# Optimization experiments

Measured on AMD Instinct MI355X. Metric: run time of the kernel, lower is better.

The kernel has to match this reference:

```python
import jax, jax.numpy as jnp
import numpy as np

BS, QLEN, KLEN = 2, 64, 64
N_HEADS, D_KV = 8, 64
INNER = N_HEADS * D_KV  # 512
VOCAB = 4096


def _layernorm(x, g, b, eps=1e-6):
    m = jnp.mean(x, axis=-1, keepdims=True)
    v = jnp.mean(jnp.square(x - m), axis=-1, keepdims=True)
    return (x - m) * jax.lax.rsqrt(v + eps) * g + b


def _l2norm(x, eps=1e-12):
    sq = jnp.sum(jnp.square(x), axis=-1, keepdims=True)
    return x * jax.lax.rsqrt(jnp.maximum(sq, eps))


def setup_inputs() -> dict:
    key = jax.random.key(0)
    ks = jax.random.split(key, 8)
    d = {
        'query': jax.random.normal(ks[0], (BS, QLEN, INNER), jnp.float32),
        'key': jax.random.normal(ks[1], (BS, KLEN, INNER), jnp.float32),
        'q_position_embeddings': jax.random.normal(ks[2], (BS, QLEN, INNER), jnp.float32),
        'k_position_embeddings': jax.random.normal(ks[3], (BS, KLEN, INNER), jnp.float32),
        'wi_w': jax.random.normal(ks[4], (2 * INNER, INNER), jnp.float32) / np.sqrt(2 * INNER),
        'vq_dict': jax.random.normal(ks[5], (VOCAB, D_KV), jnp.float32) * np.sqrt(2.0 / (VOCAB + D_KV)),
        'vq_ln_g': jnp.ones((D_KV,), jnp.float32),
        'vq_ln_b': jnp.zeros((D_KV,), jnp.float32),
        'vq_o_w': jax.random.normal(ks[6], (D_KV, D_KV), jnp.float32) / np.sqrt(D_KV),
        'ln_g': jnp.ones((D_KV,), jnp.float32),
        'ln_b': jnp.zeros((D_KV,), jnp.float32),
    }
    return d


def reference(query, key, q_position_embeddings, k_position_embeddings,
              wi_w, vq_dict, vq_ln_g, vq_ln_b, vq_o_w, ln_g, ln_b):
    bs, qlen, dim = query.shape
    klen = key.shape[1]

    q = query + q_position_embeddings
    k = key + k_position_embeddings
    # wi(concat([q, 0])) == q @ wi_w[:dim]; wi(concat([0, k])) == k @ wi_w[dim:]
    q_proj = jnp.einsum('bqd,de->bqe', q, wi_w[:dim])   # [bs, qlen, inner]
    k_proj = jnp.einsum('bkd,de->bke', k, wi_w[dim:])   # [bs, klen, inner]

    # pairwise outer sum -> [bs, qlen, klen, inner] -> tokens of size d_kv
    rcr = q_proj[:, :, None, :] + k_proj[:, None, :, :]
    y = rcr.reshape(bs, qlen * klen * N_HEADS, D_KV)

    # --- VectorQuantizer (eval mode: no dropout, loss = 0) ---
    y_n = _l2norm(y)
    d_n = _l2norm(vq_dict)
    sim = jnp.einsum('bnd,vd->bnv', y_n, d_n)           # [bs, N, vocab]
    word_idx = jnp.argmax(sim, axis=-1)                 # [bs, N] int
    word_sim = jnp.max(sim, axis=-1)                    # [bs, N]
    z = vq_dict[word_idx]                               # gather
    emb = jax.lax.stop_gradient(z - y) + y              # straight-through
    emb = _layernorm(emb, vq_ln_g, vq_ln_b)
    emb = jnp.einsum('bnd,de->bne', emb, vq_o_w)

    r3 = emb.reshape(bs, qlen, klen, N_HEADS, D_KV)
    r3_scores = word_sim.reshape(bs, qlen, klen, N_HEADS, 1)
    out_ids = word_idx.reshape(bs, qlen, klen, N_HEADS, 1)

    r3_weighted = jnp.mean(r3 * r3_scores, axis=2)      # [bs, qlen, n_heads, d_kv]
    r3_weighted = jnp.transpose(r3_weighted, (0, 2, 1, 3))  # [bs, n_heads, qlen, d_kv]
    r3_weighted = _layernorm(r3_weighted, ln_g, ln_b)
    return r3_weighted, out_ids, r3_scores
```

## Files before the change

kernel.cpp:

```cpp
#include <hip/hip_runtime.h>
#include <math.h>

#define BS 2
#define QLEN 64
#define KLEN 64
#define NH 8
#define DKV 64
#define INNER 512
#define VOCAB 4096
#define CHUNKV 64
#define RS 130
#define BUFD (CHUNKV * RS)

typedef double vdbl4 __attribute__((ext_vector_type(4)));
typedef double vdbl2 __attribute__((ext_vector_type(2)));


__global__ __launch_bounds__(256) void k_prep(
    const float* __restrict__ q_in, const float* __restrict__ k_in,
    const float* __restrict__ qpe, const float* __restrict__ kpe,
    const float* __restrict__ wi,
    const float* __restrict__ vq, const float* __restrict__ g,
    const float* __restrict__ bta, const float* __restrict__ ow,
    double* __restrict__ qp, double* __restrict__ kp,
    double* __restrict__ dnt, float* __restrict__ E,
    unsigned long long* __restrict__ bestf)
{
    __shared__ double S[1600];
    __shared__ float Osh[4096];
    int bid = blockIdx.x;
    int t = threadIdx.x;

    if (bid < 1024) {
        int side = bid >> 9;
        int b    = (bid >> 8) & 1;
        int rp   = (bid >> 3) & 31;
        int cb   = bid & 7;
        const float* xin = side ? k_in : q_in;
        const float* pin = side ? kpe : qpe;
        double* outp = side ? kp : qp;
        int wrow0 = side ? INNER : 0;
        int r0 = rp * 2;
        double* xs = S;
        double* red = S + 1024;
        for (int i = t; i < 2 * INNER; i += 256) {
            int rr = i >> 9, dd = i & 511;
            int gidx = (b * 64 + r0 + rr) * INNER + dd;
            xs[rr * INNER + dd] = (double)xin[gidx] + (double)pin[gidx];
        }
        __syncthreads();
        int col = cb * 64 + (t & 63);
        int dh = t >> 6;
        double a0 = 0.0, a1 = 0.0;
        #pragma unroll 8
        for (int d = dh * 128; d < dh * 128 + 128; ++d) {
            double w = (double)wi[(size_t)(wrow0 + d) * INNER + col];
            a0 = fma(xs[d], w, a0);
            a1 = fma(xs[INNER + d], w, a1);
        }
        red[(dh * 2 + 0) * 64 + (t & 63)] = a0;
        red[(dh * 2 + 1) * 64 + (t & 63)] = a1;
        __syncthreads();
        if (t < 128) {
            int rr = t >> 6, c2 = t & 63;
            double s = (red[(0 * 2 + rr) * 64 + c2] + red[(1 * 2 + rr) * 64 + c2])
                     + (red[(2 * 2 + rr) * 64 + c2] + red[(3 * 2 + rr) * 64 + c2]);
            outp[(size_t)(b * 64 + r0 + rr) * INNER + cb * 64 + c2] = s;
        }
    } else {
        int db = bid - 1024;
        if (db < 256) bestf[db * 256 + t] = 0ull;
        double* Lsh = S;
        double* Dsh = S + 256;
        int vb = db * 4;
        int wv = t >> 6, lane = t & 63;
        for (int i = t; i < 4096; i += 256) Osh[i] = ow[i];
        int v = vb + wv;
        double z = (double)vq[v * DKV + lane];
        double s2 = z * z, s1 = z;
        for (int m = 32; m >= 1; m >>= 1) { s2 += __shfl_xor(s2, m); s1 += __shfl_xor(s1, m); }
        Dsh[lane * 5 + wv] = z * (1.0 / sqrt(fmax(s2, 1e-12)));
        double mean = s1 * (1.0 / 64.0);
        double d0 = z - mean;
        double vv2 = d0 * d0;
        for (int m = 32; m >= 1; m >>= 1) vv2 += __shfl_xor(vv2, m);
        vv2 *= (1.0 / 64.0);
        Lsh[wv * 64 + lane] = d0 * (1.0 / sqrt(vv2 + 1e-6)) * (double)g[lane] + (double)bta[lane];
        __syncthreads();
        double c0 = 0.0, c1 = 0.0, c2 = 0.0, c3 = 0.0;
        #pragma unroll 4
        for (int gg = 0; gg < 16; ++gg) {
            int jj = gg * 4;
            c0 = fma(Lsh[wv * 64 + jj + 0], (double)Osh[(jj + 0) * 64 + lane], c0);
            c1 = fma(Lsh[wv * 64 + jj + 1], (double)Osh[(jj + 1) * 64 + lane], c1);
            c2 = fma(Lsh[wv * 64 + jj + 2], (double)Osh[(jj + 2) * 64 + lane], c2);
            c3 = fma(Lsh[wv * 64 + jj + 3], (double)Osh[(jj + 3) * 64 + lane], c3);
        }
        E[v * DKV + lane] = (float)((c0 + c1) + (c2 + c3));
        {
            int j = t >> 2, vloc = t & 3;
            dnt[(size_t)j * VOCAB + vb + vloc] = Dsh[j * 5 + vloc];
        }
    }
}

__global__ __launch_bounds__(1024, 4) void k_simscan(
    const double* __restrict__ qp, const double* __restrict__ kp,
    const double* __restrict__ dnt,
    unsigned long long* __restrict__ bestf)
{
    int bid = blockIdx.x;
    int bh = bid & 15, cg = bid >> 4;
    int b = bh >> 3, h = bh & 7;
    int t = threadIdx.x;
    int w = t >> 6, l = t & 63;

    __shared__ double S[2 * BUFD];
    __shared__ int sem[8];

    int asub = l >> 4;
    int lrow = l & 15;
    bool isprod = (w < 8);

    if (t < 8) sem[t] = 0;

    int drow[4], dcol[4];
    {
        vdbl4 prow = (vdbl4){0.0, 0.0, 0.0, 0.0};
        vdbl4 pcol = (vdbl4){0.0, 0.0, 0.0, 0.0};
        double a_row = (asub == 0) ? (double)lrow : 0.0;
        double b_one = (asub == 0) ? 1.0 : 0.0;
        double a_one = (asub == 0) ? 1.0 : 0.0;
        double b_col = (asub == 0) ? (double)lrow : 0.0;
        prow = __builtin_amdgcn_mfma_f64_16x16x4f64(a_row, b_one, prow, 0, 0, 0);
        pcol = __builtin_amdgcn_mfma_f64_16x16x4f64(a_one, b_col, pcol, 0, 0, 0);
        #pragma unroll
        for (int r = 0; r < 4; ++r) { drow[r] = (int)prow[r]; dcol[r] = (int)pcol[r]; }
    }

    double afr[16];
    if (isprod) {
        const double* src = (w < 4) ? qp : kp;
        int arow = (w & 3) * 16 + lrow;
        #pragma unroll
        for (int ks = 0; ks < 16; ++ks)
            afr[ks] = src[(size_t)(b * 64 + arow) * INNER + h * 64 + ks * 4 + asub];
    }

    int ci = t - 512;
    int qg = ci & 15, kg = (ci >> 4) & 31;
    double best[4][2];
    #pragma unroll
    for (int i = 0; i < 4; ++i)
        #pragma unroll
        for (int j = 0; j < 2; ++j) best[i][j] = 0.0;

    __syncthreads();

    if (isprod) {
        for (int step = 0; step < 4; ++step) {
            if (step >= 2) {
                for (;;) {
                    int c0 = 0;
                    if (l == 0) c0 = atomicAdd(&sem[4 + step - 2], 0);
                    if (__shfl(c0, 0) >= 8) break;
                    __builtin_amdgcn_s_sleep(2);
                }
            }
            int v0 = (cg * 4 + step) * CHUNKV;
            double* buf = S + (step & 1) * BUFD;
            vdbl4 acc[4];
            #pragma unroll
            for (int vt = 0; vt < 4; ++vt) acc[vt] = (vdbl4){0.0, 0.0, 0.0, 0.0};
            size_t base = (size_t)asub * VOCAB + v0 + lrow;
            double bcur[4], bnext[4];
            #pragma unroll
            for (int vt = 0; vt < 4; ++vt) bcur[vt] = dnt[base + vt * 16];
            #pragma unroll
            for (int ks = 0; ks < 16; ++ks) {
                if (ks < 15) {
                    size_t krow = base + (size_t)((ks + 1) * 4) * VOCAB;
                    #pragma unroll
                    for (int vt = 0; vt < 4; ++vt) bnext[vt] = dnt[krow + vt * 16];
                }
                #pragma unroll
                for (int vt = 0; vt < 4; ++vt)
                    acc[vt] = __builtin_amdgcn_mfma_f64_16x16x4f64(
                        afr[ks], bcur[vt], acc[vt], 0, 0, 0);
                if (ks < 15) {
                    #pragma unroll
                    for (int vt = 0; vt < 4; ++vt) bcur[vt] = bnext[vt];
                }
            }
            bool isq = (w < 4);
            #pragma unroll
            for (int vt = 0; vt < 4; ++vt)
                #pragma unroll
                for (int r = 0; r < 4; ++r) {
                    int vl = vt * 16 + dcol[r];
                    int grow = (w & 3) * 16 + drow[r];
                    int slot = isq ? ((grow & 15) * 4 + (grow >> 4))
                                   : (64 + (grow & 31) * 2 + (grow >> 5));
                    unsigned long long code =
                        (unsigned long long)((4095 - (v0 + vl)) << 1);
                    double s = fma(acc[vt][r], 1.0 / 64.0, 1.5);
                    unsigned long long bb2 = __double_as_longlong(s) & ~0x1FFFull;
                    if (isq) bb2 |= code;
                    buf[vl * RS + slot] = __longlong_as_double(bb2);
                }
            __threadfence_block();
            if (l == 0) atomicAdd(&sem[step], 1);
        }
    } else {
        for (int step = 0; step < 4; ++step) {
            for (;;) {
                int c0 = 0;
                if (l == 0) c0 = atomicAdd(&sem[step], 0);
                if (__shfl(c0, 0) >= 8) break;
                __builtin_amdgcn_s_sleep(2);
            }
            double* buf = S + (step & 1) * BUFD;
            #pragma unroll 2
            for (int v = 0; v < CHUNKV; ++v) {
                vdbl2 q01 = *(const vdbl2*)&buf[v * RS + qg * 4];
                vdbl2 q23 = *(const vdbl2*)&buf[v * RS + qg * 4 + 2];
                vdbl2 k01 = *(const vdbl2*)&buf[v * RS + 64 + kg * 2];
                best[0][0] = fmax(best[0][0], q01[0] + k01[0]);
                best[0][1] = fmax(best[0][1], q01[0] + k01[1]);
                best[1][0] = fmax(best[1][0], q01[1] + k01[0]);
                best[1][1] = fmax(best[1][1], q01[1] + k01[1]);
                best[2][0] = fmax(best[2][0], q23[0] + k01[0]);
                best[2][1] = fmax(best[2][1], q23[0] + k01[1]);
                best[3][0] = fmax(best[3][0], q23[1] + k01[0]);
                best[3][1] = fmax(best[3][1], q23[1] + k01[1]);
            }
            __threadfence_block();
            if (l == 0) atomicAdd(&sem[4 + step], 1);
        }
        #pragma unroll
        for (int i = 0; i < 4; ++i)
            #pragma unroll
            for (int j = 0; j < 2; ++j) {
                int q = qg + 16 * i, k = kg + 32 * j;
                atomicMax(&bestf[((size_t)bh * 64 + q) * 64 + k],
                          (unsigned long long)__double_as_longlong(best[i][j]));
            }
    }
}

__global__ __launch_bounds__(256) void k_combine(
    const unsigned long long* __restrict__ bestf,
    const double* __restrict__ qp, const double* __restrict__ kp,
    const float* __restrict__ E,
    const float* __restrict__ lng, const float* __restrict__ lnb,
    float* __restrict__ out)
{
    int bid = blockIdx.x;
    int bh = bid & 15, q = bid >> 4;
    int b = bh >> 3, h = bh & 7;
    int t = threadIdx.x;
    int w = t >> 6, lane = t & 63;

    __shared__ double qrow[64];
    __shared__ double gpart[4][64];
    __shared__ double knpart[4][64];
    __shared__ double qnpart[4];
    __shared__ float  ws_l[64];
    __shared__ int    idx_l[64];
    __shared__ float  epart[4][64];

    if (t < 64) qrow[t] = qp[(size_t)(b * 64 + q) * INNER + h * 64 + t];
    __syncthreads();

    {
        const double* krow = kp + (size_t)(b * 64 + lane) * INNER + h * 64 + w * 16;
        double gd = 0.0, kn = 0.0;
        #pragma unroll
        for (int i = 0; i < 16; ++i) {
            double xk = krow[i];
            gd = fma(qrow[w * 16 + i], xk, gd);
            kn = fma(xk, xk, kn);
        }
        gpart[w][lane] = gd;
        knpart[w][lane] = kn;
        if (lane == 0) {
            double qn = 0.0;
            #pragma unroll
            for (int i = 0; i < 16; ++i) { double xq = qrow[w * 16 + i]; qn = fma(xq, xq, qn); }
            qnpart[w] = qn;
        }
    }
    __syncthreads();

    if (w == 0) {
        int k = lane;
        double gdot = (gpart[0][k] + gpart[1][k]) + (gpart[2][k] + gpart[3][k]);
        double kn2  = (knpart[0][k] + knpart[1][k]) + (knpart[2][k] + knpart[3][k]);
        double qn2  = (qnpart[0] + qnpart[1]) + (qnpart[2] + qnpart[3]);
        unsigned long long bb = bestf[((size_t)bh * 64 + q) * 64 + k];
        int vidx = 4095 - (int)(bb & 0xFFFull);
        double sval = __longlong_as_double(bb & ~0x1FFFull);
        double tru = (sval - 3.0) * 64.0;
        double n2 = qn2 + kn2 + 2.0 * gdot;
        double wsim = tru * (1.0 / sqrt(fmax(n2, 1e-12)));
        size_t oidx = ((size_t)(b * QLEN + q) * KLEN + k) * NH + h;
        out[65536 + oidx] = (float)vidx;
        out[131072 + oidx] = (float)wsim;
        ws_l[k] = (float)wsim;
        idx_l[k] = vidx;
    }
    __syncthreads();

    {
        int d = lane;
        float acc = 0.0f;
        #pragma unroll 4
        for (int k2 = w * 16; k2 < w * 16 + 16; ++k2)
            acc += E[idx_l[k2] * DKV + d] * ws_l[k2];
        epart[w][d] = acc;
    }
    __syncthreads();

    if (w == 0) {
        int d = lane;
        float acc = ((epart[0][d] + epart[1][d]) + (epart[2][d] + epart[3][d])) * (1.0f / 64.0f);
        float mean = acc;
        for (int m = 32; m >= 1; m >>= 1) mean += __shfl_xor(mean, m);
        mean *= (1.0f / 64.0f);
        float dv = acc - mean;
        float var = dv * dv;
        for (int m = 32; m >= 1; m >>= 1) var += __shfl_xor(var, m);
        var *= (1.0f / 64.0f);
        float o = dv * rsqrtf(var + 1e-6f) * lng[d] + lnb[d];
        out[(((size_t)b * NH + h) * QLEN + q) * DKV + d] = o;
    }
}

extern "C" void kernel_launch(void* const* d_in, const int* in_sizes, int n_in,
                              void* d_out, int out_size, void* d_ws, size_t ws_size,
                              hipStream_t stream) {
    const float* query = (const float*)d_in[0];
    const float* key   = (const float*)d_in[1];
    const float* qpe   = (const float*)d_in[2];
    const float* kpe   = (const float*)d_in[3];
    const float* wi    = (const float*)d_in[4];
    const float* vq    = (const float*)d_in[5];
    const float* vqg   = (const float*)d_in[6];
    const float* vqb   = (const float*)d_in[7];
    const float* ow    = (const float*)d_in[8];
    const float* lng   = (const float*)d_in[9];
    const float* lnb   = (const float*)d_in[10];
    float* out = (float*)d_out;

    char* ws = (char*)d_ws;
    double* qp  = (double*)(ws + 0);
    double* kp  = (double*)(ws + 524288);
    double* dnt = (double*)(ws + 1048576);
    float*  E   = (float*) (ws + 3145728);
    unsigned long long* bestf = (unsigned long long*)(ws + 4194304);

    k_prep   <<<2048, 256, 0, stream>>>(query, key, qpe, kpe, wi, vq, vqg, vqb, ow,
                                        qp, kp, dnt, E, bestf);
    k_simscan<<<256, 1024, 0, stream>>>(qp, kp, dnt, bestf);
    k_combine<<<1024, 256, 0, stream>>>(bestf, qp, kp, E, lng, lnb, out);
}
```

Before: 153.1 us.

## Retile simscan consumer to 8x4 register tiles with vocab split and shared-memory reduction

Consumer threads in the similarity-scan kernel now each own an 8x4 (q,k) register tile over a quarter of each vocab chunk, instead of a 4x2 tile over the whole chunk. The producer's shared-memory slot layout is permuted and rotated to match the new read pattern. The goal is fewer LDS loads per max-add and less bank conflicting. The four vocab-slice partial maxima are then reduced through shared memory with an extra semaphore stage before the global atomicMax. This adds a serialized reduction tail and a larger register footprint (32 doubles) per consumer thread.

```diff
diff --git a/kernel.cpp b/kernel.cpp
--- a/kernel.cpp
+++ b/kernel.cpp
@@ -116,13 +116,13 @@
     int w = t >> 6, l = t & 63;
 
     __shared__ double S[2 * BUFD];
-    __shared__ int sem[8];
+    __shared__ int sem[9];
 
     int asub = l >> 4;
     int lrow = l & 15;
     bool isprod = (w < 8);
 
-    if (t < 8) sem[t] = 0;
+    if (t < 9) sem[t] = 0;
 
     int drow[4], dcol[4];
     {
@@ -148,12 +148,18 @@
     }
 
     int ci = t - 512;
-    int qg = ci & 15, kg = (ci >> 4) & 31;
-    double best[4][2];
+    int qi = ci & 7;
+    int kb = (ci >> 3) & 15;
+    int vs = ci >> 7;
+    int qo[4];
     #pragma unroll
-    for (int i = 0; i < 4; ++i)
+    for (int r = 0; r < 4; ++r) qo[r] = (4 * qi + ((r + qi) & 3)) * 2;
+    int ko0 = 64 + 4 * kb;
+    double best[8][4];
+    #pragma unroll
+    for (int a = 0; a < 8; ++a)
         #pragma unroll
-        for (int j = 0; j < 2; ++j) best[i][j] = 0.0;
+        for (int b2 = 0; b2 < 4; ++b2) best[a][b2] = 0.0;
 
     __syncthreads();
 
@@ -199,8 +205,13 @@
                 for (int r = 0; r < 4; ++r) {
                     int vl = vt * 16 + dcol[r];
                     int grow = (w & 3) * 16 + drow[r];
-                    int slot = isq ? ((grow & 15) * 4 + (grow >> 4))
-                                   : (64 + (grow & 31) * 2 + (grow >> 5));
+                    int slot;
+                    if (isq) {
+                        int qi8 = grow >> 3, rr = (grow >> 1) & 3;
+                        slot = (4 * qi8 + ((rr + qi8) & 3)) * 2 + (grow & 1);
+                    } else {
+                        slot = 64 + grow;
+                    }
                     unsigned long long code =
                         (unsigned long long)((4095 - (v0 + vl)) << 1);
                     double s = fma(acc[vt][r], 1.0 / 64.0, 1.5);
@@ -219,32 +230,61 @@
                 if (__shfl(c0, 0) >= 8) break;
                 __builtin_amdgcn_s_sleep(2);
             }
-            double* buf = S + (step & 1) * BUFD;
+            const double* row = S + (step & 1) * BUFD + vs * 16 * RS;
             #pragma unroll 2
-            for (int v = 0; v < CHUNKV; ++v) {
-                vdbl2 q01 = *(const vdbl2*)&buf[v * RS + qg * 4];
-                vdbl2 q23 = *(const vdbl2*)&buf[v * RS + qg * 4 + 2];
-                vdbl2 k01 = *(const vdbl2*)&buf[v * RS + 64 + kg * 2];
-                best[0][0] = fmax(best[0][0], q01[0] + k01[0]);
-                best[0][1] = fmax(best[0][1], q01[0] + k01[1]);
-                best[1][0] = fmax(best[1][0], q01[1] + k01[0]);
-                best[1][1] = fmax(best[1][1], q01[1] + k01[1]);
-                best[2][0] = fmax(best[2][0], q23[0] + k01[0]);
-                best[2][1] = fmax(best[2][1], q23[0] + k01[1]);
-                best[3][0] = fmax(best[3][0], q23[1] + k01[0]);
-                best[3][1] = fmax(best[3][1], q23[1] + k01[1]);
+            for (int vi = 0; vi < 16; ++vi, row += RS) {
+                vdbl2 q0 = *(const vdbl2*)(row + qo[0]);
+                vdbl2 q1 = *(const vdbl2*)(row + qo[1]);
+                vdbl2 q2 = *(const vdbl2*)(row + qo[2]);
+                vdbl2 q3 = *(const vdbl2*)(row + qo[3]);
+                vdbl2 k0 = *(const vdbl2*)(row + ko0);
+                vdbl2 k1 = *(const vdbl2*)(row + ko0 + 2);
+                double qa[8] = {q0[0], q0[1], q1[0], q1[1],
+                                q2[0], q2[1], q3[0], q3[1]};
+                double kv0 = k0[0], kv1 = k0[1], kv2 = k1[0], kv3 = k1[1];
+                #pragma unroll
+                for (int a = 0; a < 8; ++a) {
+                    best[a][0] = fmax(best[a][0], qa[a] + kv0);
+                    best[a][1] = fmax(best[a][1], qa[a] + kv1);
+                    best[a][2] = fmax(best[a][2], qa[a] + kv2);
+                    best[a][3] = fmax(best[a][3], qa[a] + kv3);
+                }
             }
             __threadfence_block();
             if (l == 0) atomicAdd(&sem[4 + step], 1);
         }
+        for (;;) {
+            int c0 = 0;
+            if (l == 0) c0 = atomicAdd(&sem[7], 0);
+            if (__shfl(c0, 0) >= 8) break;
+            __builtin_amdgcn_s_sleep(2);
+        }
+        double* red = S;
         #pragma unroll
-        for (int i = 0; i < 4; ++i)
-            #pragma unroll
-            for (int j = 0; j < 2; ++j) {
-                int q = qg + 16 * i, k = kg + 32 * j;
+        for (int a = 0; a < 8; ++a)
+            #pragma unroll
+            for (int b2 = 0; b2 < 4; ++b2)
+                red[(a * 4 + b2) * 512 + ci] = best[a][b2];
+        __threadfence_block();
+        if (l == 0) atomicAdd(&sem[8], 1);
+        if (ci < 128) {
+            for (;;) {
+                int c0 = 0;
+                if (l == 0) c0 = atomicAdd(&sem[8], 0);
+                if (__shfl(c0, 0) >= 8) break;
+                __builtin_amdgcn_s_sleep(2);
+            }
+            #pragma unroll
+            for (int j = 0; j < 32; ++j) {
+                double m0 = fmax(red[j * 512 + ci], red[j * 512 + ci + 128]);
+                double m1 = fmax(red[j * 512 + ci + 256], red[j * 512 + ci + 384]);
+                double m = fmax(m0, m1);
+                int q = qi * 8 + (j >> 2);
+                int k = kb * 4 + (j & 3);
                 atomicMax(&bestf[((size_t)bh * 64 + q) * 64 + k],
-                          (unsigned long long)__double_as_longlong(best[i][j]));
-            }
+                          (unsigned long long)__double_as_longlong(m));
+            }
+        }
     }
 }
 
```

Result: slower. 168.7 us (+10.2%).
